# Performance work log

Measured on AMD Instinct MI355X. Metric: run time of the kernel, lower is better.

The kernel has to match this reference:

```python
import jax, jax.numpy as jnp
import numpy as np

B_, L_, D_ = 2, 4096, 1024
E_ = 2
DI = E_ * D_            # 2048
H_ = 16
HD_ = DI // H_          # 128
N_ = 128
K_ = 4                  # d_conv
CS_ = 256               # SSD chunk size
MC_ = 256               # Hebbian memory chunk size
ALPHA = 0.5             # memory_alpha (== write_alpha default)


def _silu(x):
    return x * jax.nn.sigmoid(x)


def _rmsnorm(x, w, eps=1e-6):
    return x * jax.lax.rsqrt(jnp.mean(x * x, axis=-1, keepdims=True) + eps) * w


def setup_inputs() -> dict:
    key = jax.random.key(0)
    ks = jax.random.split(key, 8)
    proj_dim = 2 * DI + 2 * H_ * N_ + H_
    n = lambda k, sh, sc: jax.random.normal(k, sh, jnp.float32) * sc
    return {
        "x": n(ks[0], (B_, L_, D_), 1.0),
        "norm_w": jnp.ones((D_,), jnp.float32),
        "w_in": n(ks[1], (proj_dim, D_), 0.02),
        "conv_w": n(ks[2], (DI, K_), 0.2),
        "conv_b": jnp.zeros((DI,), jnp.float32),
        "A_log": jnp.log(2.0 * jnp.ones((H_,), jnp.float32)),
        "dt_bias": jnp.zeros((H_,), jnp.float32),
        "D_skip": jnp.ones((DI,), jnp.float32),
        "w_out": n(ks[3], (D_, DI), 0.02),
        "w_write": n(ks[4], (D_, D_), 0.02),
        "w_read": n(ks[5], (D_, D_), 0.02),
        "decay": jnp.float32(4.6),
    }


def _forward(x, norm_w, w_in, conv_w, conv_b, A_log, dt_bias, D_skip,
             w_out, w_write, w_read, decay):
    B, L, D = x.shape
    residual = x
    xn = _rmsnorm(x, norm_w)

    # ---- SSDBlock ----
    proj = xn @ w_in.T  # (B,L,2*DI+2*H*N+H)
    val = proj[..., :DI]
    gate = proj[..., DI:2 * DI]
    Bp = proj[..., 2 * DI:2 * DI + H_ * N_].reshape(B, L, H_, N_)
    Cp = proj[..., 2 * DI + H_ * N_:2 * DI + 2 * H_ * N_].reshape(B, L, H_, N_)
    dt = jax.nn.softplus(proj[..., -H_:] + dt_bias)  # (B,L,H)

    # causal depthwise conv1d (kernel K_, groups=DI)
    vp = jnp.pad(val, ((0, 0), (K_ - 1, 0), (0, 0)))
    val = sum(conv_w[:, k] * vp[:, k:k + L, :] for k in range(K_)) + conv_b
    val = _silu(val).reshape(B, L, H_, HD_)

    ld = dt * (-jnp.exp(A_log))  # log decay (B,L,H)

    nc = L // CS_
    to_chunks = lambda a: jnp.moveaxis(a.reshape(B, nc, CS_, *a.shape[2:]), 1, 0)
    tril = jnp.tril(jnp.ones((CS_, CS_), bool))
    Dv = D_skip.reshape(1, H_, 1, HD_)

    def ssd_chunk(h, inp):
        v_c, b_c, c_c, ld_c = inp  # (B,CS,H,HD), (B,CS,H,N), (B,CS,H,N), (B,CS,H)
        cum = jnp.cumsum(ld_c, axis=1)            # (B,CS,H)
        cum_h = jnp.transpose(cum, (0, 2, 1))     # (B,H,CS)
        dd = cum_h[:, :, :, None] - cum_h[:, :, None, :]
        Lmat = jnp.where(tril, jnp.exp(dd), 0.0)
        M = jnp.einsum('blhn,bmhn->bhlm', c_c, b_c) * Lmat
        v_h = jnp.transpose(v_c, (0, 2, 1, 3))    # (B,H,CS,HD)
        Y = M @ v_h
        Y = Y + jnp.einsum('blhn,bhdn,blh->bhld', c_c, h, jnp.exp(cum))
        Y = Y + Dv * v_h
        h = jnp.exp(cum[:, -1])[:, :, None, None] * h + \
            jnp.einsum('blhd,blhn,blh->bhdn', v_c, b_c, jnp.exp(cum[:, -1:, :] - cum))
        return h, Y

    h0 = jnp.zeros((B, H_, HD_, N_), jnp.float32)
    _, Ys = jax.lax.scan(ssd_chunk, h0,
                         (to_chunks(val), to_chunks(Bp), to_chunks(Cp), to_chunks(ld)))
    # (nc,B,H,CS,HD) -> (B,L,DI)
    Y = jnp.transpose(Ys, (1, 0, 3, 2, 4)).reshape(B, L, DI)
    out = (Y * _silu(gate)) @ w_out.T  # (B,L,D)

    # ---- Hebbian memory (chunkwise) ----
    gamma = jax.nn.sigmoid(decay)
    lg = jnp.log(gamma)
    v = out @ w_write.T
    wk = jnp.pad(out[:, :-1], ((0, 0), (1, 0), (0, 0)))  # shifted write keys
    p = jnp.arange(MC_)
    diffs = jnp.maximum(p[:, None] - 1 - p[None, :], 0).astype(jnp.float32)
    causal = (p[:, None] > p[None, :]).astype(jnp.float32)
    Mmem = jnp.exp(diffs * lg) * causal
    gp = gamma ** p                    # read decay by position in chunk
    gw = gamma ** (MC_ - 1 - p)        # write decay to end of chunk
    nm = L // MC_
    tom = lambda a: jnp.moveaxis(a.reshape(B, nm, MC_, D), 1, 0)

    def mem_chunk(W, inp):
        rk_c, wk_c, v_c = inp  # (B,MC,D)
        inter = jnp.einsum('bde,bte->btd', W, rk_c) * gp[None, :, None]
        S = jnp.einsum('bie,bje->bij', rk_c, wk_c)
        intra = (S * Mmem) @ v_c
        W = gamma ** MC_ * W + jnp.einsum('btd,bte->bde', v_c * gw[None, :, None], wk_c)
        return W, inter + intra

    W0 = jnp.zeros((B, D, D), jnp.float32)
    _, reads = jax.lax.scan(mem_chunk, W0, (tom(out), tom(wk), tom(v)))
    reads = jnp.moveaxis(reads, 0, 1).reshape(B, L, D)
    out = out + ALPHA * (reads @ w_read.T)
    return residual + out


def reference(x, norm_w, w_in, conv_w, conv_b, A_log, dt_bias, D_skip,
              w_out, w_write, w_read, decay):
    return _forward(x, norm_w, w_in, conv_w, conv_b, A_log, dt_bias, D_skip,
                    w_out, w_write, w_read, decay)
```

## Files before the change

### kernel.cpp

```cpp
#include <hip/hip_runtime.h>
#include <hip/hip_bf16.h>

typedef __hip_bfloat16 bf16;
typedef __attribute__((ext_vector_type(8))) short short8;
typedef __attribute__((ext_vector_type(4))) float floatx4;

#define B_ 2
#define L_ 4096
#define D_ 1024
#define DI_ 2048
#define H_ 16
#define HD_ 128
#define N_ 128
#define CS_ 256
#define MC_ 256
#define NC_ 16
#define PROJ_ 8208

__device__ __forceinline__ float bf2f(short s) {
    return __uint_as_float(((unsigned)(unsigned short)s) << 16);
}

__device__ __forceinline__ void gl_lds16(const void* g, void* s) {
    __builtin_amdgcn_global_load_lds(
        (const __attribute__((address_space(1))) void*)g,
        (__attribute__((address_space(3))) void*)s, 16, 0, 0);
}

struct GemmP {
    const bf16* A; const bf16* Bt;
    float* C; bf16* CB; bf16* CB2; bf16* CB3;
    const float* add0; const float* add1; const bf16* add0b; const float* scr;
    long lda, ldb, ldc;
    int M, N, K, zinner;
    long a_zo, a_zi, b_zo, b_zi, c_zo, c_zi;
};

template<int EPI>
__global__ __launch_bounds__(256, 2) void gemm_bt(GemmP p)
{
    int z = blockIdx.z;
    int zo = z / p.zinner, zi = z % p.zinner;
    const bf16* A  = p.A  + (long)zo * p.a_zo + (long)zi * p.a_zi;
    const bf16* Bt = p.Bt + (long)zo * p.b_zo + (long)zi * p.b_zi;
    long coff = (long)zo * p.c_zo + (long)zi * p.c_zi;

    __shared__ __align__(16) bf16 As[128 * 64];
    __shared__ __align__(16) bf16 Bs[128 * 64];

    int nbx = gridDim.x, nby = gridDim.y;
    int pid = blockIdx.y * nbx + blockIdx.x;
    const int GRP = 8;
    int span = GRP * nbx;
    int grp = pid / span;
    int first = grp * GRP;
    int gsz = min(GRP, nby - first);
    int pin = pid - grp * span;
    int pid_m = first + pin % gsz;
    int pid_n = pin / gsz;
    int m0 = pid_m * 128, n0 = pid_n * 128;

    int tid = threadIdx.x;
    int lane = tid & 63, wave = tid >> 6;
    int wm = (wave >> 1) * 64, wn = (wave & 1) * 64;
    int r16 = lane & 15, q8 = (lane >> 4) * 8;

    floatx4 zero4 = {0.f, 0.f, 0.f, 0.f};
    floatx4 acc[4][4];
#pragma unroll
    for (int i = 0; i < 4; i++)
#pragma unroll
        for (int j = 0; j < 4; j++) acc[i][j] = zero4;

    int lrow = lane >> 3;
    int lcol = (lane & 7) * 8;
    int wrow = wave * 32;

    for (int k0 = 0; k0 < p.K; k0 += 64) {
#pragma unroll
        for (int t = 0; t < 4; t++) {
            int row = wrow + t * 8 + lrow;
            gl_lds16(A + (long)(m0 + row) * p.lda + k0 + lcol, &As[(wrow + t * 8) * 64]);
            int bn = n0 + row; if (bn > p.N - 1) bn = p.N - 1;
            gl_lds16(Bt + (long)bn * p.ldb + k0 + lcol, &Bs[(wrow + t * 8) * 64]);
        }
        __syncthreads();
#pragma unroll
        for (int ks = 0; ks < 64; ks += 32) {
            short8 af[4], bq[4];
#pragma unroll
            for (int i = 0; i < 4; i++)
                af[i] = *(const short8*)&As[(wm + i * 16 + r16) * 64 + ks + q8];
#pragma unroll
            for (int j = 0; j < 4; j++)
                bq[j] = *(const short8*)&Bs[(wn + j * 16 + r16) * 64 + ks + q8];
#pragma unroll
            for (int i = 0; i < 4; i++)
#pragma unroll
                for (int j = 0; j < 4; j++)
                    acc[i][j] = __builtin_amdgcn_mfma_f32_16x16x32_bf16(af[i], bq[j], acc[i][j], 0, 0, 0);
        }
        __syncthreads();
    }

    int rq = (lane >> 4) * 4;
#pragma unroll
    for (int i = 0; i < 4; i++) {
#pragma unroll
        for (int j = 0; j < 4; j++) {
#pragma unroll
            for (int r = 0; r < 4; r++) {
                int gm = m0 + wm + i * 16 + rq + r;
                int gn = n0 + wn + j * 16 + r16;
                if (gm >= p.M || gn >= p.N) continue;
                float a = acc[i][j][r];
                if (EPI == 0) {
                    p.C[coff + (long)gm * p.ldc + gn] = a;
                } else if (EPI == 1) {
                    long ix = coff + (long)gm * p.ldc + gn;
                    p.C[ix] = a; p.CB[ix] = __float2bfloat16(a);
                } else if (EPI == 2) {
                    if (gn < 2048)      p.CB [(long)gm * 2048 + gn]          = __float2bfloat16(a);
                    else if (gn < 4096) p.CB2[(long)gm * 2048 + (gn - 2048)] = __float2bfloat16(a);
                    else if (gn < 8192) p.CB3[(long)gm * 4096 + (gn - 4096)] = __float2bfloat16(a);
                    else                p.C  [(long)gm * 16   + (gn - 8192)] = a;
                } else if (EPI == 3) {
                    float lg = p.scr[1];
                    float v = (gm > gn) ? a * __expf((float)(gm - 1 - gn) * lg) : 0.f;
                    p.CB[coff + (long)gm * p.ldc + gn] = __float2bfloat16(v);
                } else if (EPI == 4) {
                    long ix = coff + (long)gm * p.ldc + gn;
                    float t = a * p.scr[16 + gm] + __bfloat162float(p.add0b[ix]);
                    p.CB[ix] = __float2bfloat16(t);
                } else if (EPI == 5) {
                    long ix = (long)gm * p.ldc + gn;
                    p.C[ix] = p.add0[ix] + p.add1[ix] + 0.5f * a;
                } else if (EPI == 6) {
                    p.CB[coff + (long)gm * p.ldc + gn] = __float2bfloat16(a);
                }
            }
        }
    }
}

__global__ void k_gamma(const float* decay, float* scr)
{
    int t = threadIdx.x;
    float g = 1.f / (1.f + expf(-decay[0]));
    float lg = logf(g);
    if (t == 0) { scr[0] = g; scr[1] = lg; scr[2] = expf(256.f * lg); }
    scr[16 + t]  = expf(lg * (float)t);
    scr[272 + t] = expf(lg * (float)(255 - t));
}

__global__ void k_f2b(const float* __restrict__ s, bf16* __restrict__ d, long n4)
{
    long i = (long)blockIdx.x * 256 + threadIdx.x;
    if (i >= n4) return;
    float4 v = ((const float4*)s)[i];
    bf16* o = d + i * 4;
    o[0] = __float2bfloat16(v.x); o[1] = __float2bfloat16(v.y);
    o[2] = __float2bfloat16(v.z); o[3] = __float2bfloat16(v.w);
}

__global__ __launch_bounds__(256) void k_rmsnorm(const float* __restrict__ x,
                                                 const float* __restrict__ w,
                                                 bf16* __restrict__ o)
{
    int row = blockIdx.x, t = threadIdx.x;
    float4 xv = ((const float4*)(x + (long)row * D_))[t];
    float s = xv.x*xv.x + xv.y*xv.y + xv.z*xv.z + xv.w*xv.w;
#pragma unroll
    for (int m = 32; m > 0; m >>= 1) s += __shfl_xor(s, m, 64);
    __shared__ float ps[4];
    if ((t & 63) == 0) ps[t >> 6] = s;
    __syncthreads();
    s = ps[0] + ps[1] + ps[2] + ps[3];
    float r = rsqrtf(s * (1.f / (float)D_) + 1e-6f);
    float4 wv = ((const float4*)w)[t];
    bf16* orow = o + (long)row * D_ + t * 4;
    orow[0] = __float2bfloat16(xv.x * r * wv.x);
    orow[1] = __float2bfloat16(xv.y * r * wv.y);
    orow[2] = __float2bfloat16(xv.z * r * wv.z);
    orow[3] = __float2bfloat16(xv.w * r * wv.w);
}

__global__ void k_ld(const float* __restrict__ dtr, const float* __restrict__ dt_bias,
                     const float* __restrict__ A_log, float* __restrict__ ld)
{
    long i = (long)blockIdx.x * 256 + threadIdx.x;
    if (i >= (long)B_ * L_ * H_) return;
    int h = (int)(i & 15);
    float d = dtr[i] + dt_bias[h];
    float sp = (d > 20.f) ? d : log1pf(__expf(d));
    ld[i] = -__expf(A_log[h]) * sp;
}

__global__ __launch_bounds__(256) void k_cum(const float* __restrict__ ld,
                                             float* __restrict__ cum_g,
                                             float* __restrict__ cumlast)
{
    int bid = blockIdx.x;
    int h = bid & 15, c = (bid >> 4) & 15, b = bid >> 8;
    long rowbase = (long)b * L_ + c * CS_;
    int tid = threadIdx.x;
    __shared__ float cum_s[256];
    cum_s[tid] = ld[(rowbase + tid) * H_ + h];
    __syncthreads();
    for (int off = 1; off < 256; off <<= 1) {
        float add = (tid >= off) ? cum_s[tid - off] : 0.f;
        __syncthreads();
        cum_s[tid] += add;
        __syncthreads();
    }
    cum_g[(rowbase + tid) * H_ + h] = cum_s[tid];
    if (tid == 255) cumlast[bid] = cum_s[255];
}

__global__ void k_conv(const bf16* __restrict__ val_b, const float* __restrict__ cw,
                       const float* __restrict__ cb, bf16* __restrict__ vo)
{
    long idx = (long)blockIdx.x * 256 + threadIdx.x;
    if (idx >= (long)B_ * L_ * DI_) return;
    long row = idx >> 11; int ch = (int)(idx & 2047);
    int l = (int)(row & (L_ - 1));
    float acc = cb[ch];
#pragma unroll
    for (int k = 0; k < 4; k++) {
        int ls = l - 3 + k;
        if (ls >= 0) acc += cw[ch * 4 + k] * __bfloat162float(val_b[(row - 3 + k) * 2048 + ch]);
    }
    float s = acc / (1.f + __expf(-acc));
    vo[idx] = __float2bfloat16(s);
}

__global__ void k_vt(const bf16* __restrict__ vconv, const float* __restrict__ cum_g,
                     const float* __restrict__ cumlast, bf16* __restrict__ vT,
                     bf16* __restrict__ vTw)
{
    __shared__ bf16 tile[32][33];
    int b = blockIdx.z;
    int r0 = blockIdx.x * 32, c0 = blockIdx.y * 32;
    int tx = threadIdx.x & 31, ty = threadIdx.x >> 5;
    for (int i = 0; i < 32; i += 8)
        tile[ty + i][tx] = vconv[((long)b * L_ + r0 + ty + i) * 2048 + c0 + tx];
    __syncthreads();
    int l = r0 + tx;
    int h = c0 >> 7;
    float w = __expf(cumlast[b * 256 + (l >> 8) * 16 + h] - cum_g[((long)b * L_ + l) * 16 + h]);
    for (int i = 0; i < 32; i += 8) {
        int col = c0 + ty + i;
        long oidx = ((long)b * 2048 + col) * L_ + l;
        bf16 v = tile[tx][ty + i];
        vT[oidx] = v;
        vTw[oidx] = __float2bfloat16(__bfloat162float(v) * w);
    }
}

__global__ void k_bt(const bf16* __restrict__ bc, bf16* __restrict__ BT)
{
    __shared__ bf16 tile[32][33];
    int b = blockIdx.z;
    int r0 = blockIdx.x * 32, c0 = blockIdx.y * 32;
    int tx = threadIdx.x & 31, ty = threadIdx.x >> 5;
    for (int i = 0; i < 32; i += 8)
        tile[ty + i][tx] = bc[((long)b * L_ + r0 + ty + i) * 4096 + c0 + tx];
    __syncthreads();
    int l = r0 + tx;
    for (int i = 0; i < 32; i += 8) {
        int col = c0 + ty + i;
        BT[((long)b * 2048 + col) * L_ + l] = tile[tx][ty + i];
    }
}

__global__ __launch_bounds__(256, 2) void k_ssd_u2(
    const bf16* __restrict__ vTw, const bf16* __restrict__ BT, float* __restrict__ U)
{
    int bid = blockIdx.x;
    int h = bid & 15, c = (bid >> 4) & 15, b = bid >> 8;
    int lane = threadIdx.x & 63, wave = threadIdx.x >> 6;
    int r16 = lane & 15, q8 = (lane >> 4) * 8, rq = (lane >> 4) * 4;
    int d0 = (wave >> 1) * 64, n0 = (wave & 1) * 64;
    const bf16* vb = vTw + ((long)b * 2048 + h * 128) * L_ + c * 256;
    const bf16* bb = BT  + ((long)b * 2048 + h * 128) * L_ + c * 256;
    floatx4 zero4 = {0.f, 0.f, 0.f, 0.f};
    floatx4 acc[4][4];
#pragma unroll
    for (int i = 0; i < 4; i++)
#pragma unroll
        for (int j = 0; j < 4; j++) acc[i][j] = zero4;
#pragma unroll 2
    for (int ks = 0; ks < 8; ks++) {
        short8 af[4], bq[4];
#pragma unroll
        for (int i = 0; i < 4; i++)
            af[i] = *(const short8*)(vb + (long)(d0 + i * 16 + r16) * L_ + ks * 32 + q8);
#pragma unroll
        for (int j = 0; j < 4; j++)
            bq[j] = *(const short8*)(bb + (long)(n0 + j * 16 + r16) * L_ + ks * 32 + q8);
#pragma unroll
        for (int i = 0; i < 4; i++)
#pragma unroll
            for (int j = 0; j < 4; j++)
                acc[i][j] = __builtin_amdgcn_mfma_f32_16x16x32_bf16(af[i], bq[j], acc[i][j], 0, 0, 0);
    }
    float* up = U + (((long)c * B_ + b) * H_ + h) * 16384;
#pragma unroll
    for (int i = 0; i < 4; i++)
#pragma unroll
        for (int j = 0; j < 4; j++)
#pragma unroll
            for (int r = 0; r < 4; r++)
                up[(d0 + i * 16 + rq + r) * 128 + (n0 + j * 16 + r16)] = acc[i][j][r];
}

__global__ void k_ssd2(const float* __restrict__ U, const float* __restrict__ cumlast,
                       bf16* __restrict__ hst)
{
    long idx = (long)blockIdx.x * 256 + threadIdx.x;
    const long tot = (long)B_ * H_ * HD_ * N_;
    if (idx >= tot) return;
    int bh = (int)(idx >> 14);
    int b = bh >> 4, h = bh & 15;
    float hv = 0.f;
    for (int c = 0; c < NC_; c++) {
        hst[c * tot + idx] = __float2bfloat16(hv);
        float ef = __expf(cumlast[b * 256 + c * 16 + h]);
        hv = ef * hv + U[c * tot + idx];
    }
}

__global__ __launch_bounds__(256, 2) void k_ssd_y(
    const bf16* __restrict__ bc_b, const bf16* __restrict__ vT,
    const bf16* __restrict__ hst, const float* __restrict__ cum_g,
    const float* __restrict__ Dskip, const bf16* __restrict__ gate_b,
    bf16* __restrict__ yg)
{
    int bid = blockIdx.x;
    int h = bid & 15, c = (bid >> 4) & 15, b = bid >> 8;
    long rowbase = (long)b * L_ + c * CS_;
    int tid = threadIdx.x, lane = tid & 63, wave = tid >> 6;
    int r16 = lane & 15, q8 = (lane >> 4) * 8, rq = (lane >> 4) * 4;
    int wt = (wave >> 1) * 32, wmS = (wave & 1) * 32, wd = (wave & 1) * 64;

    __shared__ float cum_s[256];
    __shared__ __align__(16) bf16 Ss[64][72];

    cum_s[tid] = cum_g[(rowbase + tid) * H_ + h];
    __syncthreads();

    const bf16* Cb  = bc_b + rowbase * 4096 + 2048 + h * 128;
    const bf16* Bb  = bc_b + rowbase * 4096 + h * 128;
    const bf16* vTb = vT + ((long)b * 2048 + h * 128) * L_ + c * 256;
    const bf16* hp  = hst + (((long)c * B_ + b) * H_ + h) * 16384;

    floatx4 zero4 = {0.f, 0.f, 0.f, 0.f};

    for (int tt = 0; tt < 4; tt++) {
        int tbase = tt * 64;
        short8 caf[2][4];
#pragma unroll
        for (int i = 0; i < 2; i++)
#pragma unroll
            for (int ks = 0; ks < 4; ks++)
                caf[i][ks] = *(const short8*)(Cb + (long)(tbase + wt + i * 16 + r16) * 4096 + ks * 32 + q8);

        floatx4 yacc[2][4];
#pragma unroll
        for (int i = 0; i < 2; i++)
#pragma unroll
            for (int j = 0; j < 4; j++) yacc[i][j] = zero4;
#pragma unroll
        for (int ks = 0; ks < 4; ks++)
#pragma unroll
            for (int j = 0; j < 4; j++) {
                short8 hq = *(const short8*)(hp + (long)(wd + j * 16 + r16) * 128 + ks * 32 + q8);
#pragma unroll
                for (int i = 0; i < 2; i++)
                    yacc[i][j] = __builtin_amdgcn_mfma_f32_16x16x32_bf16(caf[i][ks], hq, yacc[i][j], 0, 0, 0);
            }
        float texp[2][4];
#pragma unroll
        for (int i = 0; i < 2; i++)
#pragma unroll
            for (int r = 0; r < 4; r++)
                texp[i][r] = __expf(cum_s[tbase + wt + i * 16 + rq + r]);
#pragma unroll
        for (int i = 0; i < 2; i++)
#pragma unroll
            for (int j = 0; j < 4; j++)
#pragma unroll
                for (int r = 0; r < 4; r++) yacc[i][j][r] *= texp[i][r];

        for (int mt = 0; mt <= tt; mt++) {
            int mbase = mt * 64;
            floatx4 sacc[2][2];
#pragma unroll
            for (int i = 0; i < 2; i++)
#pragma unroll
                for (int j = 0; j < 2; j++) sacc[i][j] = zero4;
#pragma unroll
            for (int ks = 0; ks < 4; ks++) {
                short8 bq[2];
#pragma unroll
                for (int j = 0; j < 2; j++)
                    bq[j] = *(const short8*)(Bb + (long)(mbase + wmS + j * 16 + r16) * 4096 + ks * 32 + q8);
#pragma unroll
                for (int i = 0; i < 2; i++)
#pragma unroll
                    for (int j = 0; j < 2; j++)
                        sacc[i][j] = __builtin_amdgcn_mfma_f32_16x16x32_bf16(caf[i][ks], bq[j], sacc[i][j], 0, 0, 0);
            }
            __syncthreads();
#pragma unroll
            for (int i = 0; i < 2; i++)
#pragma unroll
                for (int r = 0; r < 4; r++) {
                    int trow = wt + i * 16 + rq + r;
                    float ct = cum_s[tbase + trow];
#pragma unroll
                    for (int j = 0; j < 2; j++) {
                        int mcol = mbase + wmS + j * 16 + r16;
                        float val = (mcol <= tbase + trow) ? sacc[i][j][r] * __expf(ct - cum_s[mcol]) : 0.f;
                        Ss[trow][wmS + j * 16 + r16] = __float2bfloat16(val);
                    }
                }
            __syncthreads();
#pragma unroll
            for (int ks = 0; ks < 2; ks++) {
                short8 saf[2];
#pragma unroll
                for (int i = 0; i < 2; i++)
                    saf[i] = *(const short8*)&Ss[wt + i * 16 + r16][ks * 32 + q8];
#pragma unroll
                for (int j = 0; j < 4; j++) {
                    short8 vq = *(const short8*)(vTb + (long)(wd + j * 16 + r16) * L_ + mbase + ks * 32 + q8);
#pragma unroll
                    for (int i = 0; i < 2; i++)
                        yacc[i][j] = __builtin_amdgcn_mfma_f32_16x16x32_bf16(saf[i], vq, yacc[i][j], 0, 0, 0);
                }
            }
        }
#pragma unroll
        for (int i = 0; i < 2; i++)
#pragma unroll
            for (int r = 0; r < 4; r++) {
                int t = tbase + wt + i * 16 + rq + r;
                long grow = (rowbase + t) * 2048 + h * 128;
#pragma unroll
                for (int j = 0; j < 4; j++) {
                    int d = wd + j * 16 + r16;
                    float vv = __bfloat162float(vTb[(long)d * L_ + t]);
                    float y = yacc[i][j][r] + Dskip[h * 128 + d] * vv;
                    float g = __bfloat162float(gate_b[grow + d]);
                    float sg = g / (1.f + __expf(-g));
                    yg[grow + d] = __float2bfloat16(y * sg);
                }
            }
    }
}

__global__ void k_shift(const bf16* __restrict__ ob, bf16* __restrict__ wk)
{
    long idx = (long)blockIdx.x * 256 + threadIdx.x;
    if (idx >= (long)B_ * L_ * D_) return;
    int l = (int)((idx >> 10) & (L_ - 1));
    wk[idx] = (l == 0) ? __float2bfloat16(0.f) : ob[idx - D_];
}

__global__ void k_transpose(const float* __restrict__ srcg, bf16* __restrict__ dstg)
{
    __shared__ float t[32][33];
    int b = blockIdx.z;
    const float* src = srcg + (long)b * L_ * D_;
    bf16* dst = dstg + (long)b * D_ * L_;
    int r0 = blockIdx.x * 32, c0 = blockIdx.y * 32;
    int tx = threadIdx.x & 31, ty = threadIdx.x >> 5;
    for (int i = 0; i < 32; i += 8)
        t[ty + i][tx] = src[(long)(r0 + ty + i) * D_ + c0 + tx];
    __syncthreads();
    for (int i = 0; i < 32; i += 8)
        dst[(long)(c0 + ty + i) * L_ + r0 + tx] = __float2bfloat16(t[tx][ty + i]);
}

__global__ void k_trans_wkg(const float* __restrict__ outg, const float* __restrict__ scr,
                            bf16* __restrict__ dstg)
{
    __shared__ float t[32][33];
    int b = blockIdx.z;
    const float* src = outg + (long)b * L_ * D_;
    bf16* dst = dstg + (long)b * D_ * L_;
    int r0 = blockIdx.x * 32, c0 = blockIdx.y * 32;
    int tx = threadIdx.x & 31, ty = threadIdx.x >> 5;
    for (int i = 0; i < 32; i += 8) {
        int rr = r0 + ty + i;
        float g = scr[272 + (rr & 255)];
        t[ty + i][tx] = (rr == 0) ? 0.f : src[(long)(rr - 1) * D_ + c0 + tx] * g;
    }
    __syncthreads();
    for (int i = 0; i < 32; i += 8)
        dst[(long)(c0 + ty + i) * L_ + r0 + tx] = __float2bfloat16(t[tx][ty + i]);
}

__global__ void k_m2(bf16* __restrict__ UwW, const float* __restrict__ scr)
{
    long idx = (long)blockIdx.x * 256 + threadIdx.x;
    const long tot = (long)B_ * D_ * D_;
    if (idx >= tot) return;
    float gMC = scr[2];
    float w = 0.f;
    for (int c = 0; c < NC_; c++) {
        float tmp = __bfloat162float(UwW[c * tot + idx]);
        UwW[c * tot + idx] = __float2bfloat16(w);
        w = gMC * w + tmp;
    }
}

static inline int cdiv_i(long a, long b) { return (int)((a + b - 1) / b); }

static void run_gemm(hipStream_t st, int epi, const bf16* A, const bf16* Bt,
                     float* C, bf16* CB, bf16* CB2, bf16* CB3,
                     const float* add0, const float* add1, const bf16* add0b,
                     const float* scr, int M, int N, int K,
                     long lda, long ldb, long ldc, int nbatch, int zinner,
                     long a_zo, long a_zi, long b_zo, long b_zi, long c_zo, long c_zi)
{
    GemmP p;
    p.A = A; p.Bt = Bt; p.C = C; p.CB = CB; p.CB2 = CB2; p.CB3 = CB3;
    p.add0 = add0; p.add1 = add1; p.add0b = add0b; p.scr = scr;
    p.lda = lda; p.ldb = ldb; p.ldc = ldc;
    p.M = M; p.N = N; p.K = K; p.zinner = zinner;
    p.a_zo = a_zo; p.a_zi = a_zi; p.b_zo = b_zo; p.b_zi = b_zi; p.c_zo = c_zo; p.c_zi = c_zi;
    dim3 g(cdiv_i(N, 128), cdiv_i(M, 128), nbatch);
    dim3 b(256);
    switch (epi) {
        case 0: gemm_bt<0><<<g, b, 0, st>>>(p); break;
        case 1: gemm_bt<1><<<g, b, 0, st>>>(p); break;
        case 2: gemm_bt<2><<<g, b, 0, st>>>(p); break;
        case 3: gemm_bt<3><<<g, b, 0, st>>>(p); break;
        case 4: gemm_bt<4><<<g, b, 0, st>>>(p); break;
        case 5: gemm_bt<5><<<g, b, 0, st>>>(p); break;
        case 6: gemm_bt<6><<<g, b, 0, st>>>(p); break;
    }
}

extern "C" void kernel_launch(void* const* d_in, const int* in_sizes, int n_in,
                              void* d_out, int out_size, void* d_ws, size_t ws_size,
                              hipStream_t stream)
{
    const float* x       = (const float*)d_in[0];
    const float* norm_w  = (const float*)d_in[1];
    const float* w_in    = (const float*)d_in[2];
    const float* conv_w  = (const float*)d_in[3];
    const float* conv_b  = (const float*)d_in[4];
    const float* A_log   = (const float*)d_in[5];
    const float* dt_bias = (const float*)d_in[6];
    const float* D_skip  = (const float*)d_in[7];
    const float* w_out   = (const float*)d_in[8];
    const float* w_write = (const float*)d_in[9];
    const float* w_read  = (const float*)d_in[10];
    const float* decay   = (const float*)d_in[11];
    float* outp = (float*)d_out;

    const size_t SZ_SCR  = 4096;
    const size_t SZ_DT   = (size_t)B_ * L_ * H_ * 4;
    const size_t SZ_CUML = 2048;
    const size_t SZ_WOUT = (size_t)D_ * DI_ * 2;
    const size_t SZ_WSML = (size_t)D_ * D_ * 2;
    const size_t SZ_R1   = (size_t)B_ * L_ * 2048 * 2;
    const size_t SZ_R2   = SZ_R1;
    const size_t SZ_R3   = (size_t)B_ * L_ * 4096 * 2;
    const size_t SZ_R4   = (size_t)B_ * L_ * D_ * 2 + (size_t)PROJ_ * D_ * 2;
    const size_t SZ_R5   = (size_t)B_ * L_ * 2048 * 4;

    size_t o = 0;
    auto take = [&](size_t sz) { size_t r = o; o += (sz + 255) & ~(size_t)255; return r; };
    const size_t O_SCR = take(SZ_SCR);
    const size_t O_DT  = take(SZ_DT);
    const size_t O_LD  = take(SZ_DT);
    const size_t O_CUM = take(SZ_DT);
    const size_t O_CL  = take(SZ_CUML);
    const size_t O_WO  = take(SZ_WOUT);
    const size_t O_WW  = take(SZ_WSML);
    const size_t O_WR  = take(SZ_WSML);
    const size_t O_R1  = take(SZ_R1);
    const size_t O_R2  = take(SZ_R2);
    const size_t O_R3  = take(SZ_R3);
    const size_t O_R4  = take(SZ_R4);
    const size_t O_R5  = take(SZ_R5);
    const size_t NEED = o;
    if (ws_size < NEED) return;

    char* ws = (char*)d_ws;
    float* scr     = (float*)(ws + O_SCR);
    float* dt_raw  = (float*)(ws + O_DT);
    float* ld_g    = (float*)(ws + O_LD);
    float* cum_g   = (float*)(ws + O_CUM);
    float* cumlast = (float*)(ws + O_CL);
    bf16*  w_out_b   = (bf16*)(ws + O_WO);
    bf16*  w_write_b = (bf16*)(ws + O_WW);
    bf16*  w_read_b  = (bf16*)(ws + O_WR);

    bf16*  val_b   = (bf16*)(ws + O_R1);
    bf16*  vTw_g   = (bf16*)(ws + O_R1);
    bf16*  yg_b    = (bf16*)(ws + O_R1);
    bf16*  hst_b   = (bf16*)(ws + O_R1 + (size_t)B_ * L_ * D_ * 2);
    bf16*  Sm_b    = (bf16*)(ws + O_R1);
    bf16*  intra_b = (bf16*)(ws + O_R1 + (size_t)NC_ * B_ * MC_ * MC_ * 2);
    bf16*  gate_b  = (bf16*)(ws + O_R2);
    bf16*  out_b   = (bf16*)(ws + O_R2);
    bf16*  wk_b    = (bf16*)(ws + O_R2 + (size_t)B_ * L_ * D_ * 2);
    bf16*  reads_b = wk_b;
    bf16*  bc_b    = (bf16*)(ws + O_R3);
    bf16*  UwW     = (bf16*)(ws + O_R3);
    bf16*  xn_b    = (bf16*)(ws + O_R4);
    bf16*  w_in_b  = (bf16*)(ws + O_R4 + (size_t)B_ * L_ * D_ * 2);
    bf16*  vconv_b = (bf16*)(ws + O_R4);
    float* U_ssd   = (float*)(ws + O_R4);
    float* outf    = (float*)(ws + O_R4);
    bf16*  vT_g    = (bf16*)(ws + O_R5);
    bf16*  BT_g    = (bf16*)(ws + O_R5 + (size_t)B_ * L_ * 2048 * 2);
    float* vbuf    = (float*)(ws + O_R5);
    bf16*  vTm     = (bf16*)(ws + O_R5 + (size_t)B_ * L_ * D_ * 4);
    bf16*  wkgT    = (bf16*)(ws + O_R5 + (size_t)B_ * L_ * D_ * 4 + (size_t)B_ * L_ * D_ * 2);

    const long BLD  = (long)B_ * L_ * D_;
    const long BLDI = (long)B_ * L_ * DI_;

    k_gamma<<<1, 256, 0, stream>>>(decay, scr);
    k_f2b<<<cdiv_i((long)PROJ_ * D_ / 4, 256), 256, 0, stream>>>(w_in, w_in_b, (long)PROJ_ * D_ / 4);
    k_f2b<<<cdiv_i((long)D_ * DI_ / 4, 256), 256, 0, stream>>>(w_out, w_out_b, (long)D_ * DI_ / 4);
    k_f2b<<<cdiv_i((long)D_ * D_ / 4, 256), 256, 0, stream>>>(w_write, w_write_b, (long)D_ * D_ / 4);
    k_f2b<<<cdiv_i((long)D_ * D_ / 4, 256), 256, 0, stream>>>(w_read, w_read_b, (long)D_ * D_ / 4);
    k_rmsnorm<<<B_ * L_, 256, 0, stream>>>(x, norm_w, xn_b);
    run_gemm(stream, 2, xn_b, w_in_b, dt_raw, val_b, gate_b, bc_b, nullptr, nullptr, nullptr, nullptr,
             B_ * L_, PROJ_, D_, D_, D_, 0, 1, 1, 0, 0, 0, 0, 0, 0);
    k_ld<<<cdiv_i((long)B_ * L_ * H_, 256), 256, 0, stream>>>(dt_raw, dt_bias, A_log, ld_g);
    k_cum<<<B_ * NC_ * H_, 256, 0, stream>>>(ld_g, cum_g, cumlast);
    k_conv<<<cdiv_i(BLDI, 256), 256, 0, stream>>>(val_b, conv_w, conv_b, vconv_b);
    k_vt<<<dim3(L_ / 32, DI_ / 32, B_), 256, 0, stream>>>(vconv_b, cum_g, cumlast, vT_g, vTw_g);
    k_bt<<<dim3(L_ / 32, DI_ / 32, B_), 256, 0, stream>>>(bc_b, BT_g);
    k_ssd_u2<<<B_ * NC_ * H_, 256, 0, stream>>>(vTw_g, BT_g, U_ssd);
    k_ssd2<<<cdiv_i((long)B_ * H_ * HD_ * N_, 256), 256, 0, stream>>>(U_ssd, cumlast, hst_b);
    k_ssd_y<<<B_ * NC_ * H_, 256, 0, stream>>>(bc_b, vT_g, hst_b, cum_g, D_skip, gate_b, yg_b);
    run_gemm(stream, 1, yg_b, w_out_b, outf, out_b, nullptr, nullptr, nullptr, nullptr, nullptr, nullptr,
             B_ * L_, D_, DI_, DI_, DI_, D_, 1, 1, 0, 0, 0, 0, 0, 0);
    k_shift<<<cdiv_i(BLD, 256), 256, 0, stream>>>(out_b, wk_b);
    run_gemm(stream, 0, out_b, w_write_b, vbuf, nullptr, nullptr, nullptr, nullptr, nullptr, nullptr, nullptr,
             B_ * L_, D_, D_, D_, D_, D_, 1, 1, 0, 0, 0, 0, 0, 0);
    k_transpose<<<dim3(L_ / 32, D_ / 32, B_), 256, 0, stream>>>(vbuf, vTm);
    k_trans_wkg<<<dim3(L_ / 32, D_ / 32, B_), 256, 0, stream>>>(outf, scr, wkgT);
    run_gemm(stream, 6, vTm, wkgT, nullptr, UwW, nullptr, nullptr, nullptr, nullptr, nullptr, nullptr,
             D_, D_, MC_, L_, L_, D_, B_ * NC_, NC_,
             (long)D_ * L_, MC_, (long)D_ * L_, MC_, (long)D_ * D_, (long)B_ * D_ * D_);
    k_m2<<<cdiv_i((long)B_ * D_ * D_, 256), 256, 0, stream>>>(UwW, scr);
    run_gemm(stream, 3, out_b, wk_b, nullptr, Sm_b, nullptr, nullptr, nullptr, nullptr, nullptr, scr,
             MC_, MC_, D_, D_, D_, MC_, B_ * NC_, NC_,
             (long)L_ * D_, (long)MC_ * D_, (long)L_ * D_, (long)MC_ * D_,
             (long)MC_ * MC_, (long)B_ * MC_ * MC_);
    run_gemm(stream, 6, Sm_b, vTm, nullptr, intra_b, nullptr, nullptr, nullptr, nullptr, nullptr, nullptr,
             MC_, D_, MC_, MC_, L_, D_, B_ * NC_, NC_,
             (long)MC_ * MC_, (long)B_ * MC_ * MC_, (long)D_ * L_, MC_,
             (long)L_ * D_, (long)MC_ * D_);
    run_gemm(stream, 4, out_b, UwW, nullptr, reads_b, nullptr, nullptr, nullptr, nullptr, intra_b, scr,
             MC_, D_, D_, D_, D_, D_, B_ * NC_, NC_,
             (long)L_ * D_, (long)MC_ * D_, (long)D_ * D_, (long)B_ * D_ * D_,
             (long)L_ * D_, (long)MC_ * D_);
    run_gemm(stream, 5, reads_b, w_read_b, outp, nullptr, nullptr, nullptr, x, outf, nullptr, nullptr,
             B_ * L_, D_, D_, D_, D_, D_, 1, 1, 0, 0, 0, 0, 0, 0);
}
```

Measured before the change: 908.0 us.

## Swizzle GEMM LDS tiles and remap block order across XCDs

Applies an XOR swizzle to the 16-byte column groups that global_load_lds writes into LDS, and matches it when reading MFMA fragments, to cut LDS bank conflicts on the fragment reads. It also replaces the grouped block ordering with a scheme that hands each XCD a contiguous range of tiles (including across z) and groups them 8-wide, so neighbouring tiles share L2. The extra index arithmetic is small, but the remap must be exactly right for grids that are not multiples of 8.

```diff
diff --git a/kernel.cpp b/kernel.cpp
--- a/kernel.cpp
+++ b/kernel.cpp
@@ -39,7 +39,27 @@
 template<int EPI>
 __global__ __launch_bounds__(256, 2) void gemm_bt(GemmP p)
 {
-    int z = blockIdx.z;
+    int NT = gridDim.x, MT = gridDim.y;
+    long T = (long)NT * MT * gridDim.z;
+    long flat = ((long)blockIdx.z * MT + blockIdx.y) * NT + blockIdx.x;
+    int xcd = (int)(flat & 7);
+    long q = flat >> 3;
+    long Tq = T >> 3; int Tr = (int)(T & 7);
+    long tile = (long)xcd * Tq + (long)(xcd < Tr ? xcd : Tr) + q;
+    long per_z = (long)NT * MT;
+    int z = (int)(tile / per_z);
+    int t2 = (int)(tile - (long)z * per_z);
+    int FG = NT >> 3;
+    int g, width, within;
+    if (t2 < FG * MT * 8) { g = t2 / (MT * 8); width = 8; within = t2 - g * MT * 8; }
+    else                  { g = FG; width = NT - FG * 8; within = t2 - FG * MT * 8; }
+    int m_outer = within / (8 * width);
+    int hb = MT - m_outer * 8; if (hb > 8) hb = 8;
+    int inner = within - m_outer * 8 * width;
+    int n_in = inner / hb, m_in = inner - n_in * hb;
+    int m0 = (m_outer * 8 + m_in) * 128;
+    int n0 = (g * 8 + n_in) * 128;
+
     int zo = z / p.zinner, zi = z % p.zinner;
     const bf16* A  = p.A  + (long)zo * p.a_zo + (long)zi * p.a_zi;
     const bf16* Bt = p.Bt + (long)zo * p.b_zo + (long)zi * p.b_zi;
@@ -48,18 +68,6 @@
     __shared__ __align__(16) bf16 As[128 * 64];
     __shared__ __align__(16) bf16 Bs[128 * 64];
 
-    int nbx = gridDim.x, nby = gridDim.y;
-    int pid = blockIdx.y * nbx + blockIdx.x;
-    const int GRP = 8;
-    int span = GRP * nbx;
-    int grp = pid / span;
-    int first = grp * GRP;
-    int gsz = min(GRP, nby - first);
-    int pin = pid - grp * span;
-    int pid_m = first + pin % gsz;
-    int pid_n = pin / gsz;
-    int m0 = pid_m * 128, n0 = pid_n * 128;
-
     int tid = threadIdx.x;
     int lane = tid & 63, wave = tid >> 6;
     int wm = (wave >> 1) * 64, wn = (wave & 1) * 64;
@@ -73,27 +81,30 @@
         for (int j = 0; j < 4; j++) acc[i][j] = zero4;
 
     int lrow = lane >> 3;
-    int lcol = (lane & 7) * 8;
+    int lc = ((lane & 7) ^ lrow) * 8;
     int wrow = wave * 32;
+    int rx = lane & 7;
 
     for (int k0 = 0; k0 < p.K; k0 += 64) {
 #pragma unroll
         for (int t = 0; t < 4; t++) {
             int row = wrow + t * 8 + lrow;
-            gl_lds16(A + (long)(m0 + row) * p.lda + k0 + lcol, &As[(wrow + t * 8) * 64]);
+            gl_lds16(A + (long)(m0 + row) * p.lda + k0 + lc, &As[(wrow + t * 8) * 64]);
             int bn = n0 + row; if (bn > p.N - 1) bn = p.N - 1;
-            gl_lds16(Bt + (long)bn * p.ldb + k0 + lcol, &Bs[(wrow + t * 8) * 64]);
+            gl_lds16(Bt + (long)bn * p.ldb + k0 + lc, &Bs[(wrow + t * 8) * 64]);
         }
         __syncthreads();
 #pragma unroll
         for (int ks = 0; ks < 64; ks += 32) {
+            int lb = (ks >> 3) + (lane >> 4);
+            int po = ((lb ^ rx) << 3);
             short8 af[4], bq[4];
 #pragma unroll
             for (int i = 0; i < 4; i++)
-                af[i] = *(const short8*)&As[(wm + i * 16 + r16) * 64 + ks + q8];
+                af[i] = *(const short8*)&As[(wm + i * 16 + r16) * 64 + po];
 #pragma unroll
             for (int j = 0; j < 4; j++)
-                bq[j] = *(const short8*)&Bs[(wn + j * 16 + r16) * 64 + ks + q8];
+                bq[j] = *(const short8*)&Bs[(wn + j * 16 + r16) * 64 + po];
 #pragma unroll
             for (int i = 0; i < 4; i++)
 #pragma unroll
```

After: 824.3 us. 9.2% less time.
